# Performance work log

Hardware: AMD Instinct MI355X
Metric: run time of the kernel (lower is better)

The kernel has to match this reference:

```python
import jax, jax.numpy as jnp
import numpy as np

B, S, E = 2, 2048, 2048
H, KVH = 16, 4
HD = E // H          # 128
REP = H // KVH       # 4
THETA = 100000.0


def _rope_cos_sin(seqlen, head_dim, theta=THETA):
    # Faithful to precompute_pos_cis: exponent is arange(0, d, 2) (NOT divided by d)
    freqs = 1.0 / theta ** jnp.arange(0, head_dim, 2, dtype=jnp.float32)[: head_dim // 2]
    ang = jnp.outer(jnp.arange(seqlen, dtype=jnp.float32), freqs)  # (S, HD/2)
    return jnp.cos(ang), jnp.sin(ang)


def _apply_rotary(t, cos, sin):
    # t: (B, S, h, HD) -> complex pairs along last dim
    b, s, h, d = t.shape
    t = t.astype(jnp.float32).reshape(b, s, h, d // 2, 2)
    tr, ti = t[..., 0], t[..., 1]
    c = cos[None, :, None, :]
    sn = sin[None, :, None, :]
    out_r = tr * c - ti * sn
    out_i = tr * sn + ti * c
    return jnp.stack([out_r, out_i], axis=-1).reshape(b, s, h, d)


def setup_inputs() -> dict:
    key = jax.random.key(0)
    ks = jax.random.split(key, 9)
    sc_e = 1.0 / np.sqrt(E)
    return {
        "x": jax.random.normal(ks[0], (B, S, E), jnp.float32),
        "wq": jax.random.normal(ks[1], (E, H * HD), jnp.float32) * sc_e,
        "bq": jax.random.normal(ks[2], (H * HD,), jnp.float32) * 0.01,
        "wk": jax.random.normal(ks[3], (E, KVH * HD), jnp.float32) * sc_e,
        "bk": jax.random.normal(ks[4], (KVH * HD,), jnp.float32) * 0.01,
        "wv": jax.random.normal(ks[5], (E, KVH * HD), jnp.float32) * sc_e,
        "bv": jax.random.normal(ks[6], (KVH * HD,), jnp.float32) * 0.01,
        "wo": jax.random.normal(ks[7], (H * HD, E), jnp.float32) * sc_e,
        "bo": jax.random.normal(ks[8], (E,), jnp.float32) * 0.01,
    }


def reference(x, wq, bq, wk, bk, wv, bv, wo, bo):
    b, s, _ = x.shape
    xq = (x @ wq + bq).reshape(b, s, H, HD)
    xk = (x @ wk + bk).reshape(b, s, KVH, HD)
    xv = (x @ wv + bv).reshape(b, s, KVH, HD)

    cos, sin = _rope_cos_sin(s, HD)
    xq = _apply_rotary(xq, cos, sin)
    xk = _apply_rotary(xk, cos, sin)

    # GQA: group query heads over shared KV heads instead of materializing repeat_kv
    q = xq.transpose(0, 2, 1, 3).reshape(b, KVH, REP, s, HD)  # (B, G, R, S, D)
    k = xk.transpose(0, 2, 1, 3)                               # (B, G, S, D)
    v = xv.astype(jnp.float32).transpose(0, 2, 1, 3)           # (B, G, S, D)

    scores = jnp.einsum("bgrqd,bgkd->bgrqk", q, k) / jnp.sqrt(jnp.float32(HD))
    causal = jnp.tril(jnp.ones((s, s), dtype=bool))
    scores = jnp.where(causal[None, None, None], scores, jnp.float32(-jnp.inf))
    attn = jax.nn.softmax(scores, axis=-1)
    out = jnp.einsum("bgrqk,bgkd->bgrqd", attn, v)  # (B, G, R, S, D)
    out = out.reshape(b, H, s, HD).transpose(0, 2, 1, 3).reshape(b, s, H * HD)
    return out @ wo + bo
```

## Files before the change

### kernel.cpp

```cpp
#include <hip/hip_runtime.h>
#include <math.h>

#define BB 2
#define SS 2048
#define EE 2048
#define HH 16
#define KVH 4
#define HD 128

typedef __attribute__((ext_vector_type(8))) short short8;
typedef __attribute__((ext_vector_type(4))) float f32x4;

__device__ __forceinline__ short f2b(float f) {
  unsigned u = __float_as_uint(f);
  unsigned r = (u + 0x7fffu + ((u >> 16) & 1u)) >> 16;
  return (short)r;
}

__device__ __forceinline__ void async_load16(const void* g, void* l) {
  __builtin_amdgcn_global_load_lds(
      (const __attribute__((address_space(1))) void*)g,
      (__attribute__((address_space(3))) void*)l, 16, 0, 0);
}

__device__ __forceinline__ float rope_freq(int jp) {
  return exp2f(-(float)(2 * jp) * 16.609640474436812f);
}

__global__ void f32_to_bf16(const float* __restrict__ in, short* __restrict__ out) {
  int i = (blockIdx.x * 256 + threadIdx.x) * 8;
  float4 a = *(const float4*)(in + i);
  float4 b = *(const float4*)(in + i + 4);
  short8 c;
  c[0] = f2b(a.x); c[1] = f2b(a.y); c[2] = f2b(a.z); c[3] = f2b(a.w);
  c[4] = f2b(b.x); c[5] = f2b(b.y); c[6] = f2b(b.z); c[7] = f2b(b.w);
  *(short8*)(out + i) = c;
}

__global__ void transpose_f2b(const float* __restrict__ in, short* __restrict__ out,
                              int K, int N) {
  __shared__ short tile[32][33];
  int n0 = blockIdx.x * 32, k0 = blockIdx.y * 32;
  int tx = threadIdx.x, ty = threadIdx.y;
#pragma unroll
  for (int i = 0; i < 32; i += 8)
    tile[ty + i][tx] = f2b(in[(size_t)(k0 + ty + i) * N + n0 + tx]);
  __syncthreads();
#pragma unroll
  for (int i = 0; i < 32; i += 8)
    out[(size_t)(n0 + ty + i) * K + k0 + tx] = tile[tx][ty + i];
}

__global__ __launch_bounds__(256) void gemm_qkv(
    const short* __restrict__ A, const short* __restrict__ Bt,
    const float* __restrict__ bq, const float* __restrict__ bk,
    const float* __restrict__ bv,
    short* __restrict__ qbuf, short* __restrict__ kbuf, short* __restrict__ vtr) {
  __shared__ __align__(16) short Sm[128 * 136];
  short* Al = Sm;
  short* Bl = Sm + 128 * 64;
  const int K = EE;
  int t = threadIdx.x, lane = t & 63, w = t >> 6;
  int wm = (w >> 1) * 64, wn = (w & 1) * 64;
  int m0 = blockIdx.x * 128, n0 = blockIdx.y * 128;
  const short* Ab = A + (size_t)m0 * K;
  const short* Bb = Bt + (size_t)n0 * K;
  int srow = t >> 3, scol = (t & 7) * 8;
  int lj = lane & 15, lr = lane >> 4;
  f32x4 acc[4][4] = {};
  for (int k0 = 0; k0 < K; k0 += 64) {
#pragma unroll
    for (int q = 0; q < 4; q++) {
      async_load16(Ab + (size_t)(q * 32 + srow) * K + k0 + scol,
                   (char*)Al + q * 4096 + w * 1024);
      async_load16(Bb + (size_t)(q * 32 + srow) * K + k0 + scol,
                   (char*)Bl + q * 4096 + w * 1024);
    }
    __syncthreads();
    short8 a0[4], a1[4], b0[4], b1[4];
#pragma unroll
    for (int i = 0; i < 4; i++) {
      a0[i] = *(const short8*)&Al[(wm + i * 16 + lj) * 64 + lr * 8];
      a1[i] = *(const short8*)&Al[(wm + i * 16 + lj) * 64 + 32 + lr * 8];
    }
#pragma unroll
    for (int j = 0; j < 4; j++) {
      b0[j] = *(const short8*)&Bl[(wn + j * 16 + lj) * 64 + lr * 8];
      b1[j] = *(const short8*)&Bl[(wn + j * 16 + lj) * 64 + 32 + lr * 8];
    }
#pragma unroll
    for (int i = 0; i < 4; i++)
#pragma unroll
      for (int j = 0; j < 4; j++) {
        acc[i][j] = __builtin_amdgcn_mfma_f32_16x16x32_bf16(a0[i], b0[j], acc[i][j], 0, 0, 0);
        acc[i][j] = __builtin_amdgcn_mfma_f32_16x16x32_bf16(a1[i], b1[j], acc[i][j], 0, 0, 0);
      }
    __syncthreads();
  }
  if (n0 < 2048) {
#pragma unroll
    for (int j = 0; j < 4; j++) {
      int d = wn + j * 16 + lj;
      float bias = bq[n0 + d];
      float freq = rope_freq(d >> 1);
      bool odd = (d & 1) != 0;
#pragma unroll
      for (int i = 0; i < 4; i++)
#pragma unroll
        for (int r = 0; r < 4; r++) {
          int mloc = wm + i * 16 + lr * 4 + r;
          int s = (m0 + mloc) & (SS - 1);
          float val = acc[i][j][r] + bias;
          float other = __shfl_xor(val, 1, 64);
          float ang = (float)s * freq;
          float cs = cosf(ang), sn = sinf(ang);
          float res = odd ? (other * sn + val * cs) : (val * cs - other * sn);
          Sm[mloc * 136 + d] = f2b(res);
        }
    }
  } else if (n0 < 2560) {
    int base = n0 - 2048;
#pragma unroll
    for (int j = 0; j < 4; j++) {
      int d = wn + j * 16 + lj;
      float bias = bk[base + d];
      float freq = rope_freq(d >> 1);
      bool odd = (d & 1) != 0;
#pragma unroll
      for (int i = 0; i < 4; i++)
#pragma unroll
        for (int r = 0; r < 4; r++) {
          int mloc = wm + i * 16 + lr * 4 + r;
          int s = (m0 + mloc) & (SS - 1);
          float val = acc[i][j][r] + bias;
          float other = __shfl_xor(val, 1, 64);
          float ang = (float)s * freq;
          float cs = cosf(ang), sn = sinf(ang);
          float res = odd ? (other * sn + val * cs) : (val * cs - other * sn);
          Sm[mloc * 136 + d] = f2b(res);
        }
    }
  } else {
    int base = n0 - 2560;
#pragma unroll
    for (int j = 0; j < 4; j++) {
      int d = wn + j * 16 + lj;
      float bias = bv[base + d];
#pragma unroll
      for (int i = 0; i < 4; i++)
#pragma unroll
        for (int r = 0; r < 4; r++) {
          int mloc = wm + i * 16 + lr * 4 + r;
          Sm[d * 136 + mloc] = f2b(acc[i][j][r] + bias);
        }
    }
  }
  __syncthreads();
  int r0 = t >> 4, ch = t & 15;
  if (n0 < 2048) {
#pragma unroll
    for (int p = 0; p < 8; p++) {
      int row = p * 16 + r0;
      *(short8*)(qbuf + (size_t)(m0 + row) * 2048 + n0 + ch * 8) =
          *(const short8*)&Sm[row * 136 + ch * 8];
    }
  } else if (n0 < 2560) {
    int kvh = (n0 - 2048) >> 7;
    int b = m0 >> 11, s0 = m0 & (SS - 1);
    short* dst = kbuf + ((size_t)(b * KVH + kvh) * SS + s0) * HD;
#pragma unroll
    for (int p = 0; p < 8; p++) {
      int row = p * 16 + r0;
      *(short8*)(dst + (size_t)row * HD + ch * 8) = *(const short8*)&Sm[row * 136 + ch * 8];
    }
  } else {
    int kvh = (n0 - 2560) >> 7;
    int b = m0 >> 11, s0 = m0 & (SS - 1);
    short* dst = vtr + ((size_t)(b * KVH + kvh) * HD) * SS + s0;
#pragma unroll
    for (int p = 0; p < 8; p++) {
      int row = p * 16 + r0;
      *(short8*)(dst + (size_t)row * SS + ch * 8) = *(const short8*)&Sm[row * 136 + ch * 8];
    }
  }
}

__global__ __launch_bounds__(256) void attn_kernel(
    const short* __restrict__ qb, const short* __restrict__ kb,
    const short* __restrict__ vt, short* __restrict__ ao) {
  __shared__ __align__(16) short Kl[64 * 128];
  __shared__ __align__(16) short Vl[128 * 64];
  __shared__ __align__(16) short Pl[4 * 16 * 64];
  int t = threadIdx.x, lane = t & 63, w = t >> 6;
  int lj = lane & 15, lr = lane >> 4;
  int qt = blockIdx.x, h = blockIdx.y, b = blockIdx.z;
  int kvh = h >> 2;
  int qb0 = qt * 64;
  const short* qbase = qb + (size_t)(b * SS) * 2048 + h * HD;
  const short* kbase = kb + (size_t)(b * KVH + kvh) * SS * HD;
  const short* vbase = vt + (size_t)(b * KVH + kvh) * HD * SS;
  short8 aq[4];
  int sq = qb0 + w * 16 + lj;
#pragma unroll
  for (int kk = 0; kk < 4; kk++)
    aq[kk] = *(const short8*)(qbase + (size_t)sq * 2048 + kk * 32 + lr * 8);
  f32x4 O[8] = {};
  const float NEG = -1e30f;
  float mrow[4] = {NEG, NEG, NEG, NEG};
  float lrow[4] = {0.f, 0.f, 0.f, 0.f};
  const float scale = 0.088388347648318447f;
  int nkt = qt + 1;
  for (int kt = 0; kt < nkt; ++kt) {
    short8 gk[4], gv[4];
#pragma unroll
    for (int i = 0; i < 4; i++) {
      gk[i] = *(const short8*)(kbase + (size_t)(kt * 64 + i * 16 + (t >> 4)) * HD + (t & 15) * 8);
      gv[i] = *(const short8*)(vbase + (size_t)(i * 32 + (t >> 3)) * SS + kt * 64 + (t & 7) * 8);
    }
#pragma unroll
    for (int i = 0; i < 4; i++) {
      *(short8*)&Kl[(i * 16 + (t >> 4)) * 128 + (t & 15) * 8] = gk[i];
      *(short8*)&Vl[(i * 32 + (t >> 3)) * 64 + (t & 7) * 8] = gv[i];
    }
    __syncthreads();
    f32x4 S[4];
#pragma unroll
    for (int nt = 0; nt < 4; nt++) {
      f32x4 sc = {};
#pragma unroll
      for (int kk = 0; kk < 4; kk++) {
        short8 bk_ = *(const short8*)&Kl[(nt * 16 + lj) * 128 + kk * 32 + lr * 8];
        sc = __builtin_amdgcn_mfma_f32_16x16x32_bf16(aq[kk], bk_, sc, 0, 0, 0);
      }
      S[nt] = sc;
    }
    int rowg = qb0 + w * 16 + lr * 4;
#pragma unroll
    for (int nt = 0; nt < 4; nt++) {
      int colg = kt * 64 + nt * 16 + lj;
#pragma unroll
      for (int r = 0; r < 4; r++) {
        float v = S[nt][r] * scale;
        if (colg > rowg + r) v = NEG;
        S[nt][r] = v;
      }
    }
    float alpha[4];
#pragma unroll
    for (int r = 0; r < 4; r++) {
      float m_ = fmaxf(fmaxf(S[0][r], S[1][r]), fmaxf(S[2][r], S[3][r]));
#pragma unroll
      for (int off = 1; off < 16; off <<= 1) m_ = fmaxf(m_, __shfl_xor(m_, off, 64));
      float mn = fmaxf(mrow[r], m_);
      alpha[r] = __expf(mrow[r] - mn);
      mrow[r] = mn;
    }
    float ls[4] = {0.f, 0.f, 0.f, 0.f};
#pragma unroll
    for (int nt = 0; nt < 4; nt++)
#pragma unroll
      for (int r = 0; r < 4; r++) {
        float p = __expf(S[nt][r] - mrow[r]);
        ls[r] += p;
        Pl[(w * 16 + lr * 4 + r) * 64 + nt * 16 + lj] = f2b(p);
      }
#pragma unroll
    for (int r = 0; r < 4; r++) {
      float s_ = ls[r];
#pragma unroll
      for (int off = 1; off < 16; off <<= 1) s_ += __shfl_xor(s_, off, 64);
      lrow[r] = lrow[r] * alpha[r] + s_;
    }
#pragma unroll
    for (int jt = 0; jt < 8; jt++)
#pragma unroll
      for (int r = 0; r < 4; r++) O[jt][r] *= alpha[r];
#pragma unroll
    for (int kk = 0; kk < 2; kk++) {
      short8 ap = *(const short8*)&Pl[(w * 16 + lj) * 64 + kk * 32 + lr * 8];
#pragma unroll
      for (int jt = 0; jt < 8; jt++) {
        short8 bv_ = *(const short8*)&Vl[(jt * 16 + lj) * 64 + kk * 32 + lr * 8];
        O[jt] = __builtin_amdgcn_mfma_f32_16x16x32_bf16(ap, bv_, O[jt], 0, 0, 0);
      }
    }
    __syncthreads();
  }
  size_t obase = (size_t)(b * SS + qb0 + w * 16) * 2048 + h * HD;
#pragma unroll
  for (int jt = 0; jt < 8; jt++)
#pragma unroll
    for (int r = 0; r < 4; r++) {
      int row = lr * 4 + r;
      ao[obase + (size_t)row * 2048 + jt * 16 + lj] = f2b(O[jt][r] / lrow[r]);
    }
}

__global__ __launch_bounds__(256) void gemm_out(
    const short* __restrict__ A, const short* __restrict__ Bt,
    const float* __restrict__ bo, float* __restrict__ out) {
  __shared__ __align__(16) short Al[128 * 32];
  __shared__ __align__(16) short Bl[128 * 32];
  const int K = EE;
  int t = threadIdx.x, lane = t & 63, w = t >> 6;
  int wm = (w >> 1) * 64, wn = (w & 1) * 64;
  int m0 = blockIdx.x * 128, n0 = blockIdx.y * 128;
  const short* Ab = A + (size_t)m0 * K;
  const short* Bb = Bt + (size_t)n0 * K;
  int sr = t >> 2, sc = (t & 3) * 8;
  char* AlB = (char*)Al + w * 1024;
  char* BlB = (char*)Bl + w * 1024;
  f32x4 acc[4][4] = {};
  for (int k0 = 0; k0 < K; k0 += 32) {
    async_load16(Ab + (size_t)sr * K + k0 + sc, AlB);
    async_load16(Ab + (size_t)(64 + sr) * K + k0 + sc, AlB + 4096);
    async_load16(Bb + (size_t)sr * K + k0 + sc, BlB);
    async_load16(Bb + (size_t)(64 + sr) * K + k0 + sc, BlB + 4096);
    __syncthreads();
    short8 a[4], b[4];
#pragma unroll
    for (int i = 0; i < 4; i++)
      a[i] = *(const short8*)&Al[(wm + i * 16 + (lane & 15)) * 32 + (lane >> 4) * 8];
#pragma unroll
    for (int j = 0; j < 4; j++)
      b[j] = *(const short8*)&Bl[(wn + j * 16 + (lane & 15)) * 32 + (lane >> 4) * 8];
#pragma unroll
    for (int i = 0; i < 4; i++)
#pragma unroll
      for (int j = 0; j < 4; j++)
        acc[i][j] = __builtin_amdgcn_mfma_f32_16x16x32_bf16(a[i], b[j], acc[i][j], 0, 0, 0);
    __syncthreads();
  }
#pragma unroll
  for (int j = 0; j < 4; j++) {
    int n = n0 + wn + j * 16 + (lane & 15);
    float bias = bo[n];
#pragma unroll
    for (int i = 0; i < 4; i++)
#pragma unroll
      for (int r = 0; r < 4; r++) {
        int m = m0 + wm + i * 16 + (lane >> 4) * 4 + r;
        out[(size_t)m * 2048 + n] = acc[i][j][r] + bias;
      }
  }
}

extern "C" void kernel_launch(void* const* d_in, const int* in_sizes, int n_in,
                              void* d_out, int out_size, void* d_ws, size_t ws_size,
                              hipStream_t stream) {
  const float* x  = (const float*)d_in[0];
  const float* wq = (const float*)d_in[1];
  const float* bq = (const float*)d_in[2];
  const float* wk = (const float*)d_in[3];
  const float* bk = (const float*)d_in[4];
  const float* wv = (const float*)d_in[5];
  const float* bv = (const float*)d_in[6];
  const float* wo = (const float*)d_in[7];
  const float* bo = (const float*)d_in[8];
  float* out = (float*)d_out;

  short* W1t = (short*)d_ws;
  short* Wot = W1t + (size_t)3072 * 2048;
  short* qb_ = Wot + (size_t)2048 * 2048;
  short* kb_ = qb_ + (size_t)4096 * 2048;
  short* vt_ = kb_ + (size_t)4096 * 512;
  short* ao_ = vt_ + (size_t)4096 * 512;
  short* xb_ = ao_;

  dim3 tb(32, 8);
  f32_to_bf16<<<4096, 256, 0, stream>>>(x, xb_);
  transpose_f2b<<<dim3(64, 64), tb, 0, stream>>>(wq, W1t, 2048, 2048);
  transpose_f2b<<<dim3(16, 64), tb, 0, stream>>>(wk, W1t + (size_t)2048 * 2048, 2048, 512);
  transpose_f2b<<<dim3(16, 64), tb, 0, stream>>>(wv, W1t + (size_t)2560 * 2048, 2048, 512);
  transpose_f2b<<<dim3(64, 64), tb, 0, stream>>>(wo, Wot, 2048, 2048);

  gemm_qkv<<<dim3(32, 24), 256, 0, stream>>>(xb_, W1t, bq, bk, bv, qb_, kb_, vt_);
  attn_kernel<<<dim3(32, 16, 2), 256, 0, stream>>>(qb_, kb_, vt_, ao_);
  gemm_out<<<dim3(32, 16), 256, 0, stream>>>(ao_, Wot, bo, out);
}
```

Measured before the change: 944.2 us.

## Double attention query tile per block and widen output GEMM K-step to 64

The attention kernel now gives each wave two 16-row query sub-tiles (128 queries per block), so every K/V tile loaded into shared memory is reused by twice as many queries, and the grid is halved. The output GEMM stages 64-wide K slices instead of 32, halving the barrier and loop overhead per MFMA. The trade-offs are more registers per thread, larger shared-memory tiles that may lower occupancy, and fewer attention blocks with coarser causal load balance.

```diff
diff --git a/kernel.cpp b/kernel.cpp
--- a/kernel.cpp
+++ b/kernel.cpp
@@ -190,26 +190,32 @@
     const short* __restrict__ vt, short* __restrict__ ao) {
   __shared__ __align__(16) short Kl[64 * 128];
   __shared__ __align__(16) short Vl[128 * 64];
-  __shared__ __align__(16) short Pl[4 * 16 * 64];
+  __shared__ __align__(16) short Pl[4 * 32 * 64];
   int t = threadIdx.x, lane = t & 63, w = t >> 6;
   int lj = lane & 15, lr = lane >> 4;
   int qt = blockIdx.x, h = blockIdx.y, b = blockIdx.z;
   int kvh = h >> 2;
-  int qb0 = qt * 64;
+  int qb0 = qt * 128;
   const short* qbase = qb + (size_t)(b * SS) * 2048 + h * HD;
   const short* kbase = kb + (size_t)(b * KVH + kvh) * SS * HD;
   const short* vbase = vt + (size_t)(b * KVH + kvh) * HD * SS;
-  short8 aq[4];
-  int sq = qb0 + w * 16 + lj;
-#pragma unroll
-  for (int kk = 0; kk < 4; kk++)
-    aq[kk] = *(const short8*)(qbase + (size_t)sq * 2048 + kk * 32 + lr * 8);
-  f32x4 O[8] = {};
+  short8 aq[2][4];
+#pragma unroll
+  for (int it = 0; it < 2; it++) {
+    int sq = qb0 + w * 32 + it * 16 + lj;
+#pragma unroll
+    for (int kk = 0; kk < 4; kk++)
+      aq[it][kk] = *(const short8*)(qbase + (size_t)sq * 2048 + kk * 32 + lr * 8);
+  }
+  f32x4 O[2][8] = {};
   const float NEG = -1e30f;
-  float mrow[4] = {NEG, NEG, NEG, NEG};
-  float lrow[4] = {0.f, 0.f, 0.f, 0.f};
+  float mrow[2][4], lrow[2][4];
+#pragma unroll
+  for (int it = 0; it < 2; it++)
+#pragma unroll
+    for (int r = 0; r < 4; r++) { mrow[it][r] = NEG; lrow[it][r] = 0.f; }
   const float scale = 0.088388347648318447f;
-  int nkt = qt + 1;
+  int nkt = 2 * qt + 2;
   for (int kt = 0; kt < nkt; ++kt) {
     short8 gk[4], gv[4];
 #pragma unroll
@@ -223,123 +229,138 @@
       *(short8*)&Vl[(i * 32 + (t >> 3)) * 64 + (t & 7) * 8] = gv[i];
     }
     __syncthreads();
-    f32x4 S[4];
-#pragma unroll
-    for (int nt = 0; nt < 4; nt++) {
-      f32x4 sc = {};
-#pragma unroll
-      for (int kk = 0; kk < 4; kk++) {
-        short8 bk_ = *(const short8*)&Kl[(nt * 16 + lj) * 128 + kk * 32 + lr * 8];
-        sc = __builtin_amdgcn_mfma_f32_16x16x32_bf16(aq[kk], bk_, sc, 0, 0, 0);
-      }
-      S[nt] = sc;
-    }
-    int rowg = qb0 + w * 16 + lr * 4;
-#pragma unroll
-    for (int nt = 0; nt < 4; nt++) {
-      int colg = kt * 64 + nt * 16 + lj;
+#pragma unroll
+    for (int it = 0; it < 2; it++) {
+      f32x4 S[4];
+#pragma unroll
+      for (int nt = 0; nt < 4; nt++) {
+        f32x4 sc = {};
+#pragma unroll
+        for (int kk = 0; kk < 4; kk++) {
+          short8 bk_ = *(const short8*)&Kl[(nt * 16 + lj) * 128 + kk * 32 + lr * 8];
+          sc = __builtin_amdgcn_mfma_f32_16x16x32_bf16(aq[it][kk], bk_, sc, 0, 0, 0);
+        }
+        S[nt] = sc;
+      }
+      int rowg = qb0 + w * 32 + it * 16 + lr * 4;
+#pragma unroll
+      for (int nt = 0; nt < 4; nt++) {
+        int colg = kt * 64 + nt * 16 + lj;
+#pragma unroll
+        for (int r = 0; r < 4; r++) {
+          float v = S[nt][r] * scale;
+          if (colg > rowg + r) v = NEG;
+          S[nt][r] = v;
+        }
+      }
+      float alpha[4];
 #pragma unroll
       for (int r = 0; r < 4; r++) {
-        float v = S[nt][r] * scale;
-        if (colg > rowg + r) v = NEG;
-        S[nt][r] = v;
-      }
-    }
-    float alpha[4];
-#pragma unroll
-    for (int r = 0; r < 4; r++) {
-      float m_ = fmaxf(fmaxf(S[0][r], S[1][r]), fmaxf(S[2][r], S[3][r]));
-#pragma unroll
-      for (int off = 1; off < 16; off <<= 1) m_ = fmaxf(m_, __shfl_xor(m_, off, 64));
-      float mn = fmaxf(mrow[r], m_);
-      alpha[r] = __expf(mrow[r] - mn);
-      mrow[r] = mn;
-    }
-    float ls[4] = {0.f, 0.f, 0.f, 0.f};
-#pragma unroll
-    for (int nt = 0; nt < 4; nt++)
+        float m_ = fmaxf(fmaxf(S[0][r], S[1][r]), fmaxf(S[2][r], S[3][r]));
+#pragma unroll
+        for (int off = 1; off < 16; off <<= 1) m_ = fmaxf(m_, __shfl_xor(m_, off, 64));
+        float mn = fmaxf(mrow[it][r], m_);
+        alpha[r] = __expf(mrow[it][r] - mn);
+        mrow[it][r] = mn;
+      }
+      float ls[4] = {0.f, 0.f, 0.f, 0.f};
+#pragma unroll
+      for (int nt = 0; nt < 4; nt++)
+#pragma unroll
+        for (int r = 0; r < 4; r++) {
+          float p = __expf(S[nt][r] - mrow[it][r]);
+          ls[r] += p;
+          Pl[(w * 32 + it * 16 + lr * 4 + r) * 64 + nt * 16 + lj] = f2b(p);
+        }
 #pragma unroll
       for (int r = 0; r < 4; r++) {
-        float p = __expf(S[nt][r] - mrow[r]);
-        ls[r] += p;
-        Pl[(w * 16 + lr * 4 + r) * 64 + nt * 16 + lj] = f2b(p);
-      }
-#pragma unroll
-    for (int r = 0; r < 4; r++) {
-      float s_ = ls[r];
-#pragma unroll
-      for (int off = 1; off < 16; off <<= 1) s_ += __shfl_xor(s_, off, 64);
-      lrow[r] = lrow[r] * alpha[r] + s_;
-    }
+        float s_ = ls[r];
+#pragma unroll
+        for (int off = 1; off < 16; off <<= 1) s_ += __shfl_xor(s_, off, 64);
+        lrow[it][r] = lrow[it][r] * alpha[r] + s_;
+      }
+#pragma unroll
+      for (int jt = 0; jt < 8; jt++)
+#pragma unroll
+        for (int r = 0; r < 4; r++) O[it][jt][r] *= alpha[r];
+#pragma unroll
+      for (int kk = 0; kk < 2; kk++) {
+        short8 ap = *(const short8*)&Pl[(w * 32 + it * 16 + lj) * 64 + kk * 32 + lr * 8];
+#pragma unroll
+        for (int jt = 0; jt < 8; jt++) {
+          short8 bv_ = *(const short8*)&Vl[(jt * 16 + lj) * 64 + kk * 32 + lr * 8];
+          O[it][jt] = __builtin_amdgcn_mfma_f32_16x16x32_bf16(ap, bv_, O[it][jt], 0, 0, 0);
+        }
+      }
+    }
+    __syncthreads();
+  }
+#pragma unroll
+  for (int it = 0; it < 2; it++) {
+    size_t obase = (size_t)(b * SS + qb0 + w * 32 + it * 16) * 2048 + h * HD;
 #pragma unroll
     for (int jt = 0; jt < 8; jt++)
 #pragma unroll
-      for (int r = 0; r < 4; r++) O[jt][r] *= alpha[r];
-#pragma unroll
-    for (int kk = 0; kk < 2; kk++) {
-      short8 ap = *(const short8*)&Pl[(w * 16 + lj) * 64 + kk * 32 + lr * 8];
-#pragma unroll
-      for (int jt = 0; jt < 8; jt++) {
-        short8 bv_ = *(const short8*)&Vl[(jt * 16 + lj) * 64 + kk * 32 + lr * 8];
-        O[jt] = __builtin_amdgcn_mfma_f32_16x16x32_bf16(ap, bv_, O[jt], 0, 0, 0);
-      }
-    }
-    __syncthreads();
-  }
-  size_t obase = (size_t)(b * SS + qb0 + w * 16) * 2048 + h * HD;
-#pragma unroll
-  for (int jt = 0; jt < 8; jt++)
-#pragma unroll
-    for (int r = 0; r < 4; r++) {
-      int row = lr * 4 + r;
-      ao[obase + (size_t)row * 2048 + jt * 16 + lj] = f2b(O[jt][r] / lrow[r]);
-    }
+      for (int r = 0; r < 4; r++) {
+        int row = lr * 4 + r;
+        ao[obase + (size_t)row * 2048 + jt * 16 + lj] = f2b(O[it][jt][r] / lrow[it][r]);
+      }
+  }
 }
 
 __global__ __launch_bounds__(256) void gemm_out(
     const short* __restrict__ A, const short* __restrict__ Bt,
     const float* __restrict__ bo, float* __restrict__ out) {
-  __shared__ __align__(16) short Al[128 * 32];
-  __shared__ __align__(16) short Bl[128 * 32];
+  __shared__ __align__(16) short Sm[128 * 128];
+  short* Al = Sm;
+  short* Bl = Sm + 128 * 64;
   const int K = EE;
   int t = threadIdx.x, lane = t & 63, w = t >> 6;
   int wm = (w >> 1) * 64, wn = (w & 1) * 64;
   int m0 = blockIdx.x * 128, n0 = blockIdx.y * 128;
   const short* Ab = A + (size_t)m0 * K;
   const short* Bb = Bt + (size_t)n0 * K;
-  int sr = t >> 2, sc = (t & 3) * 8;
-  char* AlB = (char*)Al + w * 1024;
-  char* BlB = (char*)Bl + w * 1024;
+  int srow = t >> 3, scol = (t & 7) * 8;
+  int lj = lane & 15, lr = lane >> 4;
   f32x4 acc[4][4] = {};
-  for (int k0 = 0; k0 < K; k0 += 32) {
-    async_load16(Ab + (size_t)sr * K + k0 + sc, AlB);
-    async_load16(Ab + (size_t)(64 + sr) * K + k0 + sc, AlB + 4096);
-    async_load16(Bb + (size_t)sr * K + k0 + sc, BlB);
-    async_load16(Bb + (size_t)(64 + sr) * K + k0 + sc, BlB + 4096);
-    __syncthreads();
-    short8 a[4], b[4];
+  for (int k0 = 0; k0 < K; k0 += 64) {
+#pragma unroll
+    for (int q = 0; q < 4; q++) {
+      async_load16(Ab + (size_t)(q * 32 + srow) * K + k0 + scol,
+                   (char*)Al + q * 4096 + w * 1024);
+      async_load16(Bb + (size_t)(q * 32 + srow) * K + k0 + scol,
+                   (char*)Bl + q * 4096 + w * 1024);
+    }
+    __syncthreads();
+    short8 a0[4], a1[4], b0[4], b1[4];
+#pragma unroll
+    for (int i = 0; i < 4; i++) {
+      a0[i] = *(const short8*)&Al[(wm + i * 16 + lj) * 64 + lr * 8];
+      a1[i] = *(const short8*)&Al[(wm + i * 16 + lj) * 64 + 32 + lr * 8];
+    }
+#pragma unroll
+    for (int j = 0; j < 4; j++) {
+      b0[j] = *(const short8*)&Bl[(wn + j * 16 + lj) * 64 + lr * 8];
+      b1[j] = *(const short8*)&Bl[(wn + j * 16 + lj) * 64 + 32 + lr * 8];
+    }
 #pragma unroll
     for (int i = 0; i < 4; i++)
-      a[i] = *(const short8*)&Al[(wm + i * 16 + (lane & 15)) * 32 + (lane >> 4) * 8];
-#pragma unroll
-    for (int j = 0; j < 4; j++)
-      b[j] = *(const short8*)&Bl[(wn + j * 16 + (lane & 15)) * 32 + (lane >> 4) * 8];
+#pragma unroll
+      for (int j = 0; j < 4; j++) {
+        acc[i][j] = __builtin_amdgcn_mfma_f32_16x16x32_bf16(a0[i], b0[j], acc[i][j], 0, 0, 0);
+        acc[i][j] = __builtin_amdgcn_mfma_f32_16x16x32_bf16(a1[i], b1[j], acc[i][j], 0, 0, 0);
+      }
+    __syncthreads();
+  }
+#pragma unroll
+  for (int j = 0; j < 4; j++) {
+    int n = n0 + wn + j * 16 + lj;
+    float bias = bo[n];
 #pragma unroll
     for (int i = 0; i < 4; i++)
 #pragma unroll
-      for (int j = 0; j < 4; j++)
-        acc[i][j] = __builtin_amdgcn_mfma_f32_16x16x32_bf16(a[i], b[j], acc[i][j], 0, 0, 0);
-    __syncthreads();
-  }
-#pragma unroll
-  for (int j = 0; j < 4; j++) {
-    int n = n0 + wn + j * 16 + (lane & 15);
-    float bias = bo[n];
-#pragma unroll
-    for (int i = 0; i < 4; i++)
-#pragma unroll
       for (int r = 0; r < 4; r++) {
-        int m = m0 + wm + i * 16 + (lane >> 4) * 4 + r;
+        int m = m0 + wm + i * 16 + lr * 4 + r;
         out[(size_t)m * 2048 + n] = acc[i][j][r] + bias;
       }
   }
@@ -375,6 +396,6 @@
   transpose_f2b<<<dim3(64, 64), tb, 0, stream>>>(wo, Wot, 2048, 2048);
 
   gemm_qkv<<<dim3(32, 24), 256, 0, stream>>>(xb_, W1t, bq, bk, bv, qb_, kb_, vt_);
-  attn_kernel<<<dim3(32, 16, 2), 256, 0, stream>>>(qb_, kb_, vt_, ao_);
+  attn_kernel<<<dim3(16, 16, 2), 256, 0, stream>>>(qb_, kb_, vt_, ao_);
   gemm_out<<<dim3(32, 16), 256, 0, stream>>>(ao_, Wot, bo, out);
 }
```

Result: slower. 1.005 ms (+6.4%).
